# Kernel optimization log

Measured on AMD Instinct MI355X. Metric: run time of the kernel, lower is better.

The kernel has to match this reference:

```python
import jax, jax.numpy as jnp
import numpy as np

HIDDEN = 768
N_HEADS = 12
D_HEAD = 64
B, T = 4, 2048


def setup_inputs() -> dict:
    key = jax.random.key(0)
    ks = jax.random.split(key, 5)
    s = 0.02
    return {
        "x": jax.random.normal(ks[0], (B, T, HIDDEN), dtype=jnp.float32),
        "w_q": jax.random.normal(ks[1], (HIDDEN, HIDDEN), dtype=jnp.float32) * s,
        "w_k": jax.random.normal(ks[2], (HIDDEN, HIDDEN), dtype=jnp.float32) * s,
        "w_v": jax.random.normal(ks[3], (HIDDEN, HIDDEN), dtype=jnp.float32) * s,
        "w_o": jax.random.normal(ks[4], (HIDDEN, HIDDEN), dtype=jnp.float32) * s,
    }


def reference(x, w_q, w_k, w_v, w_o):
    # nn.Linear applies x @ W^T; weights here are [out, in] like torch.
    b, t, h = x.shape
    q = (x @ w_q.T).reshape(b, t, N_HEADS, D_HEAD)
    k = (x @ w_k.T).reshape(b, t, N_HEADS, D_HEAD)
    v = (x @ w_v.T).reshape(b, t, N_HEADS, D_HEAD)
    # scores: [b, heads, t, t]
    scores = jnp.einsum("bqhd,bkhd->bhqk", q, k) / jnp.sqrt(jnp.float32(D_HEAD))
    weights = jax.nn.softmax(scores, axis=-1)
    # dropout p=0.0 -> identity
    ctx = jnp.einsum("bhqk,bkhd->bqhd", weights, v).reshape(b, t, h)
    return ctx @ w_o.T
```

## Files before the change

### kernel.cpp

```cpp
#include <hip/hip_runtime.h>

#define HIDDEN 768
#define NH 12
#define DH 64
#define BB 4
#define TT 2048
#define MTOT (BB * TT)

typedef __bf16 bf16x8 __attribute__((ext_vector_type(8)));
typedef short s16x8 __attribute__((ext_vector_type(8)));
typedef float f32x4 __attribute__((ext_vector_type(4)));

__device__ __forceinline__ unsigned short f2b(float f) {
    unsigned u = __builtin_bit_cast(unsigned, f);
    u += 0x7fffu + ((u >> 16) & 1u);
    return (unsigned short)(u >> 16);
}

__device__ __forceinline__ unsigned pack_bf16(float a, float b) {
    return __builtin_amdgcn_perm(__builtin_bit_cast(unsigned, b),
                                 __builtin_bit_cast(unsigned, a), 0x07060302u);
}

typedef const __attribute__((address_space(1))) unsigned int* gas_ptr;
typedef __attribute__((address_space(3))) unsigned int* las_ptr;
__device__ __forceinline__ void gload16(const void* g, void* l) {
    __builtin_amdgcn_global_load_lds((gas_ptr)(uintptr_t)g, (las_ptr)(uintptr_t)l, 16, 0, 0);
}

__global__ __launch_bounds__(256) void cvt_all(const float* __restrict__ x,
                                               const float* __restrict__ wq,
                                               const float* __restrict__ wk,
                                               const float* __restrict__ wv,
                                               const float* __restrict__ wo,
                                               unsigned short* __restrict__ out) {
    const size_t NX8 = (size_t)MTOT * HIDDEN / 8;
    const size_t NW8 = (size_t)HIDDEN * HIDDEN / 8;
    size_t i = (size_t)blockIdx.x * 256 + threadIdx.x;
    const float* src;
    size_t off = i;
    float scale = 1.0f;
    if (i < NX8) { src = x; }
    else if (i < NX8 + NW8) { src = wq; off = i - NX8; scale = 0.18033688011112042f; }
    else if (i < NX8 + 2 * NW8) { src = wk; off = i - NX8 - NW8; }
    else if (i < NX8 + 3 * NW8) { src = wv; off = i - NX8 - 2 * NW8; }
    else { src = wo; off = i - NX8 - 3 * NW8; }
    const float4* p = (const float4*)src + off * 2;
    float4 a = p[0], b = p[1];
    union { uint4 u; unsigned short s[8]; } t;
    t.s[0] = f2b(a.x * scale); t.s[1] = f2b(a.y * scale);
    t.s[2] = f2b(a.z * scale); t.s[3] = f2b(a.w * scale);
    t.s[4] = f2b(b.x * scale); t.s[5] = f2b(b.y * scale);
    t.s[6] = f2b(b.z * scale); t.s[7] = f2b(b.w * scale);
    ((uint4*)out)[i] = t.u;
}

template <int MODE, int MROWS>
__device__ __forceinline__ void gemm_body(const unsigned short* __restrict__ A,
                                          const unsigned short* __restrict__ Bm,
                                          float* __restrict__ Cf,
                                          unsigned short* __restrict__ Cb,
                                          int mBase, int nBase, int N) {
    __shared__ __align__(16) unsigned short Al[MROWS][64];
    __shared__ __align__(16) unsigned short Bl[128][64];
    const int MT = MROWS / 32;
    const int tid = threadIdx.x;
    const int lane = tid & 63;
    const int wave = tid >> 6;
    const int quad = lane >> 4;
    const int l16 = lane & 15;
    const int mw = (wave >> 1) * (MROWS / 2);
    const int nw = (wave & 1) * 64;
    const int r8 = lane >> 3;
    const int swiz = ((lane & 7) ^ r8) * 8;
    const unsigned short* Asrc = A + (size_t)(mBase + wave * (MROWS / 4) + r8) * HIDDEN + swiz;
    const unsigned short* Bsrc = Bm + (size_t)(nBase + wave * 32 + r8) * HIDDEN + swiz;

    f32x4 acc[MT][4];
#pragma unroll
    for (int mt = 0; mt < MT; ++mt)
#pragma unroll
        for (int nt = 0; nt < 4; ++nt) acc[mt][nt] = (f32x4){0.f, 0.f, 0.f, 0.f};

    for (int kb = 0; kb < HIDDEN / 64; ++kb) {
        if (kb) __syncthreads();
#pragma unroll
        for (int i = 0; i < MROWS / 32; ++i)
            gload16(Asrc + (size_t)i * 8 * HIDDEN + kb * 64,
                    &Al[wave * (MROWS / 4) + i * 8][0]);
#pragma unroll
        for (int j = 0; j < 4; ++j)
            gload16(Bsrc + (size_t)j * 8 * HIDDEN + kb * 64, &Bl[wave * 32 + j * 8][0]);
        __syncthreads();
#pragma unroll
        for (int ks = 0; ks < 2; ++ks) {
            const int cc = ((ks * 4 + quad) ^ (l16 & 7)) * 8;
            bf16x8 af[MT], bf[4];
#pragma unroll
            for (int mt = 0; mt < MT; ++mt)
                af[mt] = *(const bf16x8*)&Al[mw + mt * 16 + l16][cc];
#pragma unroll
            for (int nt = 0; nt < 4; ++nt)
                bf[nt] = *(const bf16x8*)&Bl[nw + nt * 16 + l16][cc];
#pragma unroll
            for (int mt = 0; mt < MT; ++mt)
#pragma unroll
                for (int nt = 0; nt < 4; ++nt)
                    acc[mt][nt] = __builtin_amdgcn_mfma_f32_16x16x32_bf16(
                        af[mt], bf[nt], acc[mt][nt], 0, 0, 0);
        }
    }

#pragma unroll
    for (int mt = 0; mt < MT; ++mt)
#pragma unroll
        for (int nt = 0; nt < 4; ++nt) {
            if (MODE == 2) {
                ushort4 h;
                h.x = f2b(acc[mt][nt][0]); h.y = f2b(acc[mt][nt][1]);
                h.z = f2b(acc[mt][nt][2]); h.w = f2b(acc[mt][nt][3]);
                int m0 = mBase + mw + mt * 16 + quad * 4;
                int col = nBase + nw + nt * 16 + l16;
                *(ushort4*)&Cb[(size_t)col * MTOT + m0] = h;
            } else {
#pragma unroll
                for (int r = 0; r < 4; ++r) {
                    int row = mBase + mw + mt * 16 + quad * 4 + r;
                    int col = nBase + nw + nt * 16 + l16;
                    float v = acc[mt][nt][r];
                    if (MODE == 1)
                        Cf[(size_t)row * N + col] = v;
                    else
                        Cb[(size_t)row * N + col] = f2b(v);
                }
            }
        }
}

__global__ __launch_bounds__(256, 4) void gemm_qkv(const unsigned short* __restrict__ A,
                                                   const unsigned short* __restrict__ W0,
                                                   unsigned short* __restrict__ C0,
                                                   unsigned short* __restrict__ VT) {
    const int wsel = blockIdx.y / 6;
    const int nb = blockIdx.y % 6;
    if (wsel < 2)
        gemm_body<0, 128>(A, W0 + (size_t)wsel * HIDDEN * HIDDEN, nullptr,
                          C0 + (size_t)wsel * MTOT * HIDDEN, blockIdx.x * 128, nb * 128, HIDDEN);
    else
        gemm_body<2, 128>(A, W0 + 2 * (size_t)HIDDEN * HIDDEN, nullptr, VT,
                          blockIdx.x * 128, nb * 128, HIDDEN);
}

__global__ __launch_bounds__(256, 4) void gemm_out(const unsigned short* __restrict__ A,
                                                   const unsigned short* __restrict__ Bm,
                                                   float* __restrict__ Cf) {
    gemm_body<1, 64>(A, Bm, Cf, nullptr, blockIdx.x * 64, blockIdx.y * 128, HIDDEN);
}

__global__ __launch_bounds__(256, 3) void attn_kernel(const unsigned short* __restrict__ Qg,
                                                      const unsigned short* __restrict__ Kg,
                                                      const unsigned short* __restrict__ VTg,
                                                      unsigned short* __restrict__ Ctx) {
    __shared__ __align__(16) unsigned short Kl[2][64][64];
    __shared__ __align__(16) unsigned short Vl[2][64][64];
    __shared__ __align__(16) unsigned int Pl[4][32][16];
    const int tid = threadIdx.x;
    const int lane = tid & 63;
    const int wave = tid >> 6;
    const int quad = lane >> 4;
    const int l16 = lane & 15;
    const int qt = blockIdx.y;
    const int bh = blockIdx.x;
    const int b = bh / NH, h = bh % NH;
    const int qrow0 = b * TT + qt * 128;
    const int col0 = h * DH;

    const int srow = wave * 16 + (lane >> 3);
    const int swiz = ((lane & 7) ^ (lane >> 3)) * 8;
    const unsigned short* Ksrc = Kg + (size_t)(b * TT + srow) * HIDDEN + col0 + swiz;
    const unsigned short* Vsrc = VTg + (size_t)(col0 + srow) * MTOT + b * TT + swiz;

    auto stage = [&](int buf, int kt) {
#pragma unroll
        for (int i = 0; i < 2; ++i) {
            gload16(Ksrc + (size_t)(kt * 64 + i * 8) * HIDDEN, &Kl[buf][wave * 16 + i * 8][0]);
            gload16(Vsrc + (size_t)(i * 8) * MTOT + kt * 64, &Vl[buf][wave * 16 + i * 8][0]);
        }
    };

    bf16x8 qf[2][2];
#pragma unroll
    for (int mt = 0; mt < 2; ++mt)
#pragma unroll
        for (int ks = 0; ks < 2; ++ks)
            qf[mt][ks] = *(const bf16x8*)&Qg[(size_t)(qrow0 + wave * 32 + mt * 16 + l16) * HIDDEN +
                                             col0 + ks * 32 + quad * 8];

    s16x8 osv;
#pragma unroll
    for (int e = 0; e < 8; ++e) osv[e] = 0x3F80;
    const bf16x8 ones = __builtin_bit_cast(bf16x8, osv);

    f32x4 o[2][4];
    f32x4 lacc[2];
#pragma unroll
    for (int mt = 0; mt < 2; ++mt) {
        lacc[mt] = (f32x4){0.f, 0.f, 0.f, 0.f};
#pragma unroll
        for (int nt = 0; nt < 4; ++nt) o[mt][nt] = (f32x4){0.f, 0.f, 0.f, 0.f};
    }

    const int rx = l16 & 7;
    const int rw = (l16 >> 1) & 3;
    const f32x4 z4 = (f32x4){0.f, 0.f, 0.f, 0.f};

    stage(0, 0);
    for (int kt = 0; kt < TT / 64; ++kt) {
        __syncthreads();
        if (kt + 1 < TT / 64) stage((kt + 1) & 1, kt + 1);
        const int buf = kt & 1;

        f32x4 s[2][4];
#pragma unroll
        for (int ks = 0; ks < 2; ++ks) {
            const int cc = ((ks * 4 + quad) ^ rx) * 8;
            bf16x8 kf[4];
#pragma unroll
            for (int nt = 0; nt < 4; ++nt)
                kf[nt] = *(const bf16x8*)&Kl[buf][nt * 16 + l16][cc];
            __builtin_amdgcn_s_setprio(1);
#pragma unroll
            for (int mt = 0; mt < 2; ++mt)
#pragma unroll
                for (int nt = 0; nt < 4; ++nt)
                    s[mt][nt] = __builtin_amdgcn_mfma_f32_16x16x32_bf16(
                        kf[nt], qf[mt][ks], ks ? s[mt][nt] : z4, 0, 0, 0);
            __builtin_amdgcn_s_setprio(0);
        }

#pragma unroll
        for (int ks = 0; ks < 2; ++ks) {
#pragma unroll
            for (int mt = 0; mt < 2; ++mt) {
                const int row = mt * 16 + l16;
#pragma unroll
                for (int nt2 = 0; nt2 < 2; ++nt2) {
                    const int nt = ks * 2 + nt2;
                    float p0 = __builtin_amdgcn_exp2f(s[mt][nt][0]);
                    float p1 = __builtin_amdgcn_exp2f(s[mt][nt][1]);
                    float p2 = __builtin_amdgcn_exp2f(s[mt][nt][2]);
                    float p3 = __builtin_amdgcn_exp2f(s[mt][nt][3]);
                    uint2 w;
                    w.x = pack_bf16(p0, p1);
                    w.y = pack_bf16(p2, p3);
                    const int unit = 2 * nt2 + (quad >> 1);
                    *(uint2*)&Pl[wave][row][(((unit ^ rw) << 2) | ((quad & 1) << 1))] = w;
                }
            }

            const int cc = ((ks * 4 + quad) ^ rx) * 8;
            bf16x8 pf[2], vf[4];
#pragma unroll
            for (int nt = 0; nt < 4; ++nt)
                vf[nt] = *(const bf16x8*)&Vl[buf][nt * 16 + l16][cc];
#pragma unroll
            for (int mt = 0; mt < 2; ++mt)
                pf[mt] = *(const bf16x8*)((const char*)&Pl[wave][mt * 16 + l16][0] +
                                          ((quad ^ rw) << 4));
            __builtin_amdgcn_s_setprio(1);
#pragma unroll
            for (int mt = 0; mt < 2; ++mt)
                lacc[mt] = __builtin_amdgcn_mfma_f32_16x16x32_bf16(pf[mt], ones, lacc[mt], 0, 0, 0);
#pragma unroll
            for (int mt = 0; mt < 2; ++mt)
#pragma unroll
                for (int nt = 0; nt < 4; ++nt)
                    o[mt][nt] = __builtin_amdgcn_mfma_f32_16x16x32_bf16(pf[mt], vf[nt],
                                                                        o[mt][nt], 0, 0, 0);
            __builtin_amdgcn_s_setprio(0);
        }
    }

#pragma unroll
    for (int mt = 0; mt < 2; ++mt)
#pragma unroll
        for (int r = 0; r < 4; ++r) {
            float inv = __builtin_amdgcn_rcpf(lacc[mt][r]);
            int row = qrow0 + wave * 32 + mt * 16 + quad * 4 + r;
#pragma unroll
            for (int nt = 0; nt < 4; ++nt)
                Ctx[(size_t)row * HIDDEN + col0 + nt * 16 + l16] = f2b(o[mt][nt][r] * inv);
        }
}

extern "C" void kernel_launch(void* const* d_in, const int* in_sizes, int n_in,
                              void* d_out, int out_size, void* d_ws, size_t ws_size,
                              hipStream_t stream) {
    const float* x = (const float*)d_in[0];
    const float* wq = (const float*)d_in[1];
    const float* wk = (const float*)d_in[2];
    const float* wv = (const float*)d_in[3];
    const float* wo = (const float*)d_in[4];
    float* out = (float*)d_out;

    const size_t NX = (size_t)MTOT * HIDDEN;
    const size_t NW = (size_t)HIDDEN * HIDDEN;
    unsigned short* ws = (unsigned short*)d_ws;
    unsigned short* xb = ws;
    unsigned short* wqb = xb + NX;
    unsigned short* wob = wqb + 3 * NW;
    unsigned short* qb = wob + NW;
    unsigned short* kb = qb + NX;
    unsigned short* cb = kb + NX;
    unsigned short* vtb = cb + NX;

    cvt_all<<<(int)((NX + 4 * NW) / 8 / 256), 256, 0, stream>>>(x, wq, wk, wv, wo, xb);

    gemm_qkv<<<dim3(MTOT / 128, 18), 256, 0, stream>>>(xb, wqb, qb, vtb);

    attn_kernel<<<dim3(BB * NH, TT / 128), 256, 0, stream>>>(qb, kb, vtb, cb);

    gemm_out<<<dim3(MTOT / 64, 6), 256, 0, stream>>>(cb, wob, out);
}
```

Baseline: 197.8 us.

## Software-pipeline attention: overlap PV of previous tile with QK and exp of current

```diff
diff --git a/kernel.cpp b/kernel.cpp
--- a/kernel.cpp
+++ b/kernel.cpp
@@ -157,13 +157,13 @@
     gemm_body<1, 64>(A, Bm, Cf, nullptr, blockIdx.x * 64, blockIdx.y * 128, HIDDEN);
 }
 
-__global__ __launch_bounds__(256, 3) void attn_kernel(const unsigned short* __restrict__ Qg,
+__global__ __launch_bounds__(256, 2) void attn_kernel(const unsigned short* __restrict__ Qg,
                                                       const unsigned short* __restrict__ Kg,
                                                       const unsigned short* __restrict__ VTg,
                                                       unsigned short* __restrict__ Ctx) {
     __shared__ __align__(16) unsigned short Kl[2][64][64];
     __shared__ __align__(16) unsigned short Vl[2][64][64];
-    __shared__ __align__(16) unsigned int Pl[4][32][16];
+    __shared__ __align__(16) unsigned int Pl[2][4][32][32];
     const int tid = threadIdx.x;
     const int lane = tid & 63;
     const int wave = tid >> 6;
@@ -180,12 +180,15 @@
     const unsigned short* Ksrc = Kg + (size_t)(b * TT + srow) * HIDDEN + col0 + swiz;
     const unsigned short* Vsrc = VTg + (size_t)(col0 + srow) * MTOT + b * TT + swiz;
 
-    auto stage = [&](int buf, int kt) {
-#pragma unroll
-        for (int i = 0; i < 2; ++i) {
+    auto stageK = [&](int buf, int kt) {
+#pragma unroll
+        for (int i = 0; i < 2; ++i)
             gload16(Ksrc + (size_t)(kt * 64 + i * 8) * HIDDEN, &Kl[buf][wave * 16 + i * 8][0]);
+    };
+    auto stageV = [&](int buf, int kt) {
+#pragma unroll
+        for (int i = 0; i < 2; ++i)
             gload16(Vsrc + (size_t)(i * 8) * MTOT + kt * 64, &Vl[buf][wave * 16 + i * 8][0]);
-        }
     };
 
     bf16x8 qf[2][2];
@@ -211,14 +214,40 @@
     }
 
     const int rx = l16 & 7;
-    const int rw = (l16 >> 1) & 3;
     const f32x4 z4 = (f32x4){0.f, 0.f, 0.f, 0.f};
 
-    stage(0, 0);
+    auto pv_step = [&](int pb) {
+#pragma unroll
+        for (int ks = 0; ks < 2; ++ks) {
+            const int cc = ((ks * 4 + quad) ^ rx) * 8;
+            bf16x8 pf[2], vf[4];
+#pragma unroll
+            for (int nt = 0; nt < 4; ++nt)
+                vf[nt] = *(const bf16x8*)&Vl[pb][nt * 16 + l16][cc];
+#pragma unroll
+            for (int mt = 0; mt < 2; ++mt)
+                pf[mt] = *(const bf16x8*)((const char*)&Pl[pb][wave][mt * 16 + l16][0] +
+                                          ((((ks * 4 + quad) ^ rx) << 4)));
+            __builtin_amdgcn_s_setprio(1);
+#pragma unroll
+            for (int mt = 0; mt < 2; ++mt)
+                lacc[mt] = __builtin_amdgcn_mfma_f32_16x16x32_bf16(pf[mt], ones, lacc[mt], 0, 0, 0);
+#pragma unroll
+            for (int mt = 0; mt < 2; ++mt)
+#pragma unroll
+                for (int nt = 0; nt < 4; ++nt)
+                    o[mt][nt] = __builtin_amdgcn_mfma_f32_16x16x32_bf16(pf[mt], vf[nt],
+                                                                        o[mt][nt], 0, 0, 0);
+            __builtin_amdgcn_s_setprio(0);
+        }
+    };
+
+    stageK(0, 0);
     for (int kt = 0; kt < TT / 64; ++kt) {
         __syncthreads();
-        if (kt + 1 < TT / 64) stage((kt + 1) & 1, kt + 1);
-        const int buf = kt & 1;
+        if (kt + 1 < TT / 64) stageK((kt + 1) & 1, kt + 1);
+        stageV(kt & 1, kt);
+        const int kbuf = kt & 1;
 
         f32x4 s[2][4];
 #pragma unroll
@@ -227,7 +256,7 @@
             bf16x8 kf[4];
 #pragma unroll
             for (int nt = 0; nt < 4; ++nt)
-                kf[nt] = *(const bf16x8*)&Kl[buf][nt * 16 + l16][cc];
+                kf[nt] = *(const bf16x8*)&Kl[kbuf][nt * 16 + l16][cc];
             __builtin_amdgcn_s_setprio(1);
 #pragma unroll
             for (int mt = 0; mt < 2; ++mt)
@@ -238,48 +267,28 @@
             __builtin_amdgcn_s_setprio(0);
         }
 
-#pragma unroll
-        for (int ks = 0; ks < 2; ++ks) {
-#pragma unroll
-            for (int mt = 0; mt < 2; ++mt) {
-                const int row = mt * 16 + l16;
-#pragma unroll
-                for (int nt2 = 0; nt2 < 2; ++nt2) {
-                    const int nt = ks * 2 + nt2;
-                    float p0 = __builtin_amdgcn_exp2f(s[mt][nt][0]);
-                    float p1 = __builtin_amdgcn_exp2f(s[mt][nt][1]);
-                    float p2 = __builtin_amdgcn_exp2f(s[mt][nt][2]);
-                    float p3 = __builtin_amdgcn_exp2f(s[mt][nt][3]);
-                    uint2 w;
-                    w.x = pack_bf16(p0, p1);
-                    w.y = pack_bf16(p2, p3);
-                    const int unit = 2 * nt2 + (quad >> 1);
-                    *(uint2*)&Pl[wave][row][(((unit ^ rw) << 2) | ((quad & 1) << 1))] = w;
-                }
+        if (kt) pv_step((kt - 1) & 1);
+
+#pragma unroll
+        for (int mt = 0; mt < 2; ++mt) {
+            const int row = mt * 16 + l16;
+#pragma unroll
+            for (int nt = 0; nt < 4; ++nt) {
+                float p0 = __builtin_amdgcn_exp2f(s[mt][nt][0]);
+                float p1 = __builtin_amdgcn_exp2f(s[mt][nt][1]);
+                float p2 = __builtin_amdgcn_exp2f(s[mt][nt][2]);
+                float p3 = __builtin_amdgcn_exp2f(s[mt][nt][3]);
+                uint2 w;
+                w.x = pack_bf16(p0, p1);
+                w.y = pack_bf16(p2, p3);
+                const int unit = 2 * nt + (quad >> 1);
+                *(uint2*)&Pl[kbuf][wave][row][(((unit ^ rx) << 2) | ((quad & 1) << 1))] = w;
             }
-
-            const int cc = ((ks * 4 + quad) ^ rx) * 8;
-            bf16x8 pf[2], vf[4];
-#pragma unroll
-            for (int nt = 0; nt < 4; ++nt)
-                vf[nt] = *(const bf16x8*)&Vl[buf][nt * 16 + l16][cc];
-#pragma unroll
-            for (int mt = 0; mt < 2; ++mt)
-                pf[mt] = *(const bf16x8*)((const char*)&Pl[wave][mt * 16 + l16][0] +
-                                          ((quad ^ rw) << 4));
-            __builtin_amdgcn_s_setprio(1);
-#pragma unroll
-            for (int mt = 0; mt < 2; ++mt)
-                lacc[mt] = __builtin_amdgcn_mfma_f32_16x16x32_bf16(pf[mt], ones, lacc[mt], 0, 0, 0);
-#pragma unroll
-            for (int mt = 0; mt < 2; ++mt)
-#pragma unroll
-                for (int nt = 0; nt < 4; ++nt)
-                    o[mt][nt] = __builtin_amdgcn_mfma_f32_16x16x32_bf16(pf[mt], vf[nt],
-                                                                        o[mt][nt], 0, 0, 0);
-            __builtin_amdgcn_s_setprio(0);
         }
     }
+
+    __syncthreads();
+    pv_step((TT / 64 - 1) & 1);
 
 #pragma unroll
     for (int mt = 0; mt < 2; ++mt)
```

After: 204.5 us. 3.4% more time.
